# Performance work log

Hardware: AMD Instinct MI355X
Metric: run time of the kernel (lower is better)

The kernel has to match this reference:

```python
import jax, jax.numpy as jnp
import numpy as np

N_NODES = 100000
N_EDGES = 3200000
N_FEAT = 64
HID = 64
GDIM = 32
N_CLASS = 2
NUM_GRAPHS = 16


def setup_inputs() -> dict:
    key = jax.random.key(0)
    ks = jax.random.split(key, 24)

    def w(k, fan_in, fan_out):
        return (jax.random.normal(k, (fan_in, fan_out), jnp.float32) / np.sqrt(fan_in)).astype(jnp.float32)

    inp = {
        'x': jax.random.normal(ks[0], (N_NODES, N_FEAT), jnp.float32),
        'edge_index': jax.random.randint(ks[1], (2, N_EDGES), 0, N_NODES, jnp.int32),
        'batch': jnp.sort(jax.random.randint(ks[2], (N_NODES,), 0, NUM_GRAPHS, jnp.int32)),
        # lin0: nr_features -> nhid0
        'lin0_w': w(ks[3], N_FEAT, HID), 'lin0_b': jnp.zeros((HID,), jnp.float32),
        # SAGEConv 1: lin_l (aggregated, with bias), lin_r (self, no bias)
        's1_lw': w(ks[4], HID, HID), 's1_lb': jnp.zeros((HID,), jnp.float32), 's1_rw': w(ks[5], HID, HID),
        # SAGEConv 2
        's2_lw': w(ks[6], HID, HID), 's2_lb': jnp.zeros((HID,), jnp.float32), 's2_rw': w(ks[7], HID, HID),
        # embedding heads
        'emb0_w': w(ks[8], HID, GDIM), 'emb0_b': jnp.zeros((GDIM,), jnp.float32),
        'emb1_w': w(ks[9], HID, GDIM), 'emb1_b': jnp.zeros((GDIM,), jnp.float32),
        'emb2_w': w(ks[10], HID, GDIM), 'emb2_b': jnp.zeros((GDIM,), jnp.float32),
        'merge_w': w(ks[11], 3 * GDIM, GDIM), 'merge_b': jnp.zeros((GDIM,), jnp.float32),
        # global attention pooling: gate_nn (GDIM->1), v_nn (GDIM->GDIM)
        'gate_w': w(ks[12], GDIM, 1), 'gate_b': jnp.zeros((1,), jnp.float32),
        'v_w': w(ks[13], GDIM, GDIM), 'v_b': jnp.zeros((GDIM,), jnp.float32),
        'out_w': w(ks[14], GDIM, N_CLASS), 'out_b': jnp.zeros((N_CLASS,), jnp.float32),
    }
    return inp


def _sage(x, src, dst, lw, lb, rw):
    # mean aggregation of source features at destination nodes
    deg = jax.ops.segment_sum(jnp.ones_like(src, jnp.float32), dst, num_segments=N_NODES)
    agg = jax.ops.segment_sum(x[src], dst, num_segments=N_NODES)
    mean = agg / jnp.maximum(deg, 1.0)[:, None]
    return mean @ lw + lb + x @ rw


def reference(x, edge_index, batch,
              lin0_w, lin0_b, s1_lw, s1_lb, s1_rw, s2_lw, s2_lb, s2_rw,
              emb0_w, emb0_b, emb1_w, emb1_b, emb2_w, emb2_b,
              merge_w, merge_b, gate_w, gate_b, v_w, v_b, out_w, out_b):
    src, dst = edge_index[0], edge_index[1]
    x0 = x @ lin0_w + lin0_b                       # [N, HID]
    x1 = _sage(x0, src, dst, s1_lw, s1_lb, s1_rw)  # [N, HID]
    x2 = _sage(x1, src, dst, s2_lw, s2_lb, s2_rw)  # [N, HID]
    # eval mode: dropout = identity
    e0 = jax.nn.relu(x0 @ emb0_w + emb0_b)
    e1 = jax.nn.relu(x1 @ emb1_w + emb1_b)
    e2 = jax.nn.relu(x2 @ emb2_w + emb2_b)
    xc = jax.nn.relu(jnp.concatenate([e0, e1, e2], axis=1) @ merge_w + merge_b)  # [N, GDIM]
    # global attention pooling with per-graph softmax
    g = (xc @ gate_w + gate_b)[:, 0]               # [N]
    v = xc @ v_w + v_b                             # [N, GDIM]
    m = jax.ops.segment_max(g, batch, num_segments=NUM_GRAPHS)
    e = jnp.exp(g - m[batch])
    d = jax.ops.segment_sum(e, batch, num_segments=NUM_GRAPHS)
    a = e / d[batch]
    pooled = jax.ops.segment_sum(a[:, None] * v, batch, num_segments=NUM_GRAPHS)  # [NG, GDIM]
    logits = pooled @ out_w + out_b                # [NG, 2]
    output1 = jax.nn.softmax(logits, axis=-1)
    output2 = logits
    return (output1, output2)
```

## Files before the change

kernel.cpp:

```cpp
#include <hip/hip_runtime.h>
#include <hip/hip_bf16.h>
#include <hip/hip_fp16.h>

#define N_NODES 100000
#define N_EDGES 3200000
#define HID 64
#define GDIM 32
#define NUM_GRAPHS 16
#define NB1 256
#define BSHIFT 9
#define B1 512

__device__ __forceinline__ unsigned fkey(float f) {
    unsigned u = __float_as_uint(f);
    return (u & 0x80000000u) ? ~u : (u | 0x80000000u);
}
__device__ __forceinline__ float funkey(unsigned k) {
    unsigned u = (k & 0x80000000u) ? (k ^ 0x80000000u) : ~k;
    return __uint_as_float(u);
}

struct half4 { __half2 lo, hi; };
struct __align__(16) half8 { __half2 a, b, c, d; };

__global__ __launch_bounds__(256) void hist1_kernel(const int* __restrict__ dst, int* __restrict__ h1, int E4) {
    __shared__ int h[NB1];
    int t = threadIdx.x, b = blockIdx.x;
    h[t] = 0;
    __syncthreads();
    for (int i = b * 256 + t; i < E4; i += B1 * 256) {
        int4 d = ((const int4*)dst)[i];
        atomicAdd(&h[d.x >> BSHIFT], 1);
        atomicAdd(&h[d.y >> BSHIFT], 1);
        atomicAdd(&h[d.z >> BSHIFT], 1);
        atomicAdd(&h[d.w >> BSHIFT], 1);
    }
    __syncthreads();
    h1[b * NB1 + t] = h[t];
}

__global__ __launch_bounds__(256) void scan1_kernel(const int* __restrict__ h1, int* __restrict__ off1,
                                                    int* __restrict__ bstart, int E) {
    __shared__ int ts[256];
    int t = threadIdx.x;
    int tot = 0;
    for (int k = 0; k < B1; k++) tot += h1[k * NB1 + t];
    ts[t] = tot;
    __syncthreads();
    for (int off = 1; off < 256; off <<= 1) {
        int v = (t >= off) ? ts[t - off] : 0;
        __syncthreads();
        ts[t] += v;
        __syncthreads();
    }
    int base = ts[t] - tot;
    bstart[t] = base;
    if (t == 255) bstart[256] = E;
    int run = base;
    for (int k = 0; k < B1; k++) { off1[k * NB1 + t] = run; run += h1[k * NB1 + t]; }
}

__global__ __launch_bounds__(256) void scatter1_kernel(const int* __restrict__ src, const int* __restrict__ dst,
                                                       const int* __restrict__ off1, int* __restrict__ pairs, int E4) {
    __shared__ int cur[NB1];
    int t = threadIdx.x, b = blockIdx.x;
    cur[t] = off1[b * NB1 + t];
    __syncthreads();
    for (int i = b * 256 + t; i < E4; i += B1 * 256) {
        int4 d = ((const int4*)dst)[i];
        int4 s = ((const int4*)src)[i];
        int p0 = atomicAdd(&cur[d.x >> BSHIFT], 1);
        int p1 = atomicAdd(&cur[d.y >> BSHIFT], 1);
        int p2 = atomicAdd(&cur[d.z >> BSHIFT], 1);
        int p3 = atomicAdd(&cur[d.w >> BSHIFT], 1);
        pairs[p0] = (s.x << BSHIFT) | (d.x & 511);
        pairs[p1] = (s.y << BSHIFT) | (d.y & 511);
        pairs[p2] = (s.z << BSHIFT) | (d.z & 511);
        pairs[p3] = (s.w << BSHIFT) | (d.w & 511);
    }
}

__global__ __launch_bounds__(256) void bucket_csr_kernel(const int* __restrict__ pairs, const int* __restrict__ bstart,
                                                         int* __restrict__ rowstart, int* __restrict__ csr,
                                                         int N, int E) {
    __shared__ int hist[512];
    __shared__ int ts[256];
    int b = blockIdx.x, t = threadIdx.x;
    int estart = bstart[b], eend = bstart[b + 1];
    hist[t] = 0; hist[t + 256] = 0;
    __syncthreads();
    for (int e = estart + t; e < eend; e += 256) {
        int pr = pairs[e];
        atomicAdd(&hist[pr & 511], 1);
    }
    __syncthreads();
    int a0 = hist[2 * t], a1 = hist[2 * t + 1];
    int s = a0 + a1;
    ts[t] = s;
    __syncthreads();
    for (int off = 1; off < 256; off <<= 1) {
        int v = (t >= off) ? ts[t - off] : 0;
        __syncthreads();
        ts[t] += v;
        __syncthreads();
    }
    int excl = ts[t] - s;
    __syncthreads();
    hist[2 * t]     = estart + excl;
    hist[2 * t + 1] = estart + excl + a0;
    int nb0 = b << BSHIFT;
    int i0 = nb0 + 2 * t, i1 = i0 + 1;
    if (i0 < N) rowstart[i0] = estart + excl;
    if (i1 < N) rowstart[i1] = estart + excl + a0;
    if (b == gridDim.x - 1 && t == 0) rowstart[N] = E;
    __syncthreads();
    for (int e = estart + t; e < eend; e += 256) {
        int pr = pairs[e];
        int p = atomicAdd(&hist[pr & 511], 1);
        csr[p] = pr >> BSHIFT;
    }
}

__global__ __launch_bounds__(256) void lin0_kernel(const float* __restrict__ x, const float* __restrict__ W,
                            const float* __restrict__ b, float* __restrict__ y, __half* __restrict__ yh, int N) {
    __shared__ __align__(16) float Wl[64 * 64];
    __shared__ float bl[64];
    int t = threadIdx.x;
    for (int i = t; i < 64 * 64; i += 256) Wl[i] = W[i];
    if (t < 64) bl[t] = b[t];
    __syncthreads();
    int row = blockIdx.x * 256 + t;
    if (row >= N) return;
    float acc[64];
#pragma unroll
    for (int j = 0; j < 64; j++) acc[j] = bl[j];
    const float4* xr = (const float4*)(x + (size_t)row * 64);
#pragma unroll
    for (int c = 0; c < 16; c++) {
        float4 xv = xr[c];
        float xs[4] = {xv.x, xv.y, xv.z, xv.w};
#pragma unroll
        for (int kk = 0; kk < 4; kk++) {
            int k = c * 4 + kk;
#pragma unroll
            for (int j4 = 0; j4 < 16; j4++) {
                float4 w = *(const float4*)&Wl[k * 64 + j4 * 4];
                acc[j4 * 4 + 0] += xs[kk] * w.x;
                acc[j4 * 4 + 1] += xs[kk] * w.y;
                acc[j4 * 4 + 2] += xs[kk] * w.z;
                acc[j4 * 4 + 3] += xs[kk] * w.w;
            }
        }
    }
    float4* yr = (float4*)(y + (size_t)row * 64);
#pragma unroll
    for (int c = 0; c < 16; c++)
        yr[c] = make_float4(acc[c * 4], acc[c * 4 + 1], acc[c * 4 + 2], acc[c * 4 + 3]);
    __half2* hr = (__half2*)(yh + (size_t)row * 64);
#pragma unroll
    for (int c = 0; c < 32; c++)
        hr[c] = __halves2half2(__float2half_rn(acc[c * 2]), __float2half_rn(acc[c * 2 + 1]));
}

__global__ __launch_bounds__(256) void agg_kernel(const __half* __restrict__ xh, const int* __restrict__ rowstart,
                           const int* __restrict__ csr, float* __restrict__ meanout, int N) {
    int wid = threadIdx.x >> 6, lane = threadIdx.x & 63;
    int node = blockIdx.x * 4 + wid;
    if (node >= N) return;
    int ro = rowstart[node], re = rowstart[node + 1];
    int g = lane >> 3, c8 = lane & 7;
    float acc[8];
#pragma unroll
    for (int j = 0; j < 8; j++) acc[j] = 0.f;
    for (int base = ro; base < re; base += 64) {
        int rem = re - base;
        int idx = 0;
        if (lane < rem) idx = csr[base + lane];
        int kmax = rem < 64 ? rem : 64;
        for (int k = 0; k < kmax; k += 8) {
            int e = k + g;
            int s = __shfl(idx, e);
            if (e < kmax) {
                half8 hv = *(const half8*)(xh + (size_t)s * 64 + (c8 << 3));
                float2 f0 = __half22float2(hv.a);
                float2 f1 = __half22float2(hv.b);
                float2 f2 = __half22float2(hv.c);
                float2 f3 = __half22float2(hv.d);
                acc[0] += f0.x; acc[1] += f0.y; acc[2] += f1.x; acc[3] += f1.y;
                acc[4] += f2.x; acc[5] += f2.y; acc[6] += f3.x; acc[7] += f3.y;
            }
        }
    }
#pragma unroll
    for (int off = 8; off < 64; off <<= 1) {
#pragma unroll
        for (int j = 0; j < 8; j++) acc[j] += __shfl_xor(acc[j], off);
    }
    int deg = re - ro;
    float inv = 1.0f / (float)(deg > 0 ? deg : 1);
    if (lane < 8) {
        float4* mr = (float4*)(meanout + (size_t)node * 64 + (c8 << 3));
        mr[0] = make_float4(acc[0] * inv, acc[1] * inv, acc[2] * inv, acc[3] * inv);
        mr[1] = make_float4(acc[4] * inv, acc[5] * inv, acc[6] * inv, acc[7] * inv);
    }
}

__global__ __launch_bounds__(256) void sage_kernel(const float* __restrict__ mean, const float* __restrict__ xin,
                            const float* __restrict__ lw, const float* __restrict__ lb,
                            const float* __restrict__ rw, float* __restrict__ xout,
                            __half* __restrict__ xhout, int N) {
    __shared__ __align__(16) float LW[64 * 64];
    __shared__ __align__(16) float RW[64 * 64];
    __shared__ float LB[64];
    int t = threadIdx.x;
    for (int i = t; i < 64 * 64; i += 256) { LW[i] = lw[i]; RW[i] = rw[i]; }
    if (t < 64) LB[t] = lb[t];
    __syncthreads();
    int row = blockIdx.x * 256 + t;
    if (row >= N) return;
    float acc[64];
#pragma unroll
    for (int j = 0; j < 64; j++) acc[j] = LB[j];
    const float4* mr = (const float4*)(mean + (size_t)row * 64);
    const float4* xr = (const float4*)(xin + (size_t)row * 64);
#pragma unroll
    for (int c = 0; c < 16; c++) {
        float4 xv = mr[c];
        float xs[4] = {xv.x, xv.y, xv.z, xv.w};
#pragma unroll
        for (int kk = 0; kk < 4; kk++) {
            int k = c * 4 + kk;
#pragma unroll
            for (int j4 = 0; j4 < 16; j4++) {
                float4 w = *(const float4*)&LW[k * 64 + j4 * 4];
                acc[j4 * 4 + 0] += xs[kk] * w.x;
                acc[j4 * 4 + 1] += xs[kk] * w.y;
                acc[j4 * 4 + 2] += xs[kk] * w.z;
                acc[j4 * 4 + 3] += xs[kk] * w.w;
            }
        }
    }
#pragma unroll
    for (int c = 0; c < 16; c++) {
        float4 xv = xr[c];
        float xs[4] = {xv.x, xv.y, xv.z, xv.w};
#pragma unroll
        for (int kk = 0; kk < 4; kk++) {
            int k = c * 4 + kk;
#pragma unroll
            for (int j4 = 0; j4 < 16; j4++) {
                float4 w = *(const float4*)&RW[k * 64 + j4 * 4];
                acc[j4 * 4 + 0] += xs[kk] * w.x;
                acc[j4 * 4 + 1] += xs[kk] * w.y;
                acc[j4 * 4 + 2] += xs[kk] * w.z;
                acc[j4 * 4 + 3] += xs[kk] * w.w;
            }
        }
    }
    float4* yr = (float4*)(xout + (size_t)row * 64);
#pragma unroll
    for (int c = 0; c < 16; c++)
        yr[c] = make_float4(acc[c * 4], acc[c * 4 + 1], acc[c * 4 + 2], acc[c * 4 + 3]);
    if (xhout) {
        __half2* hr = (__half2*)(xhout + (size_t)row * 64);
#pragma unroll
        for (int c = 0; c < 32; c++)
            hr[c] = __halves2half2(__float2half_rn(acc[c * 2]), __float2half_rn(acc[c * 2 + 1]));
    }
}

__global__ __launch_bounds__(256) void head_kernel(const float* __restrict__ x0, const float* __restrict__ x1,
                            const float* __restrict__ x2, const int* __restrict__ batch,
                            const float* __restrict__ e0w, const float* __restrict__ e0b,
                            const float* __restrict__ e1w, const float* __restrict__ e1b,
                            const float* __restrict__ e2w, const float* __restrict__ e2b,
                            const float* __restrict__ mw, const float* __restrict__ mb,
                            const float* __restrict__ gw, const float* __restrict__ gbp,
                            const float* __restrict__ vw, const float* __restrict__ vb,
                            float* __restrict__ gout, float* __restrict__ vout,
                            unsigned* __restrict__ mkey, int N) {
    __shared__ __align__(16) float EW[3 * 64 * 32];
    __shared__ __align__(16) float MW[96 * 32];
    __shared__ __align__(16) float VW[32 * 32];
    __shared__ float EB[96], MB[32], GW[32], VB[32];
    __shared__ float GB;
    __shared__ unsigned smax[16];
    int t = threadIdx.x;
    for (int i = t; i < 2048; i += 256) { EW[i] = e0w[i]; EW[2048 + i] = e1w[i]; EW[4096 + i] = e2w[i]; }
    for (int i = t; i < 3072; i += 256) MW[i] = mw[i];
    for (int i = t; i < 1024; i += 256) VW[i] = vw[i];
    if (t < 32) { EB[t] = e0b[t]; EB[32 + t] = e1b[t]; EB[64 + t] = e2b[t];
                  MB[t] = mb[t]; GW[t] = gw[t]; VB[t] = vb[t]; }
    if (t == 0) GB = gbp[0];
    if (t < 16) smax[t] = 0u;
    __syncthreads();
    int node = blockIdx.x * 256 + t;
    if (node < N) {
        float xc[32];
#pragma unroll
        for (int j = 0; j < 32; j++) xc[j] = MB[j];
        const float* px[3] = {x0 + (size_t)node * 64, x1 + (size_t)node * 64, x2 + (size_t)node * 64};
        for (int h = 0; h < 3; h++) {
            float e[32];
#pragma unroll
            for (int j = 0; j < 32; j++) e[j] = EB[h * 32 + j];
            const float4* xr = (const float4*)px[h];
#pragma unroll
            for (int c = 0; c < 16; c++) {
                float4 xv = xr[c];
                float xs[4] = {xv.x, xv.y, xv.z, xv.w};
#pragma unroll
                for (int kk = 0; kk < 4; kk++) {
                    int k = c * 4 + kk;
#pragma unroll
                    for (int j4 = 0; j4 < 8; j4++) {
                        float4 w = *(const float4*)&EW[h * 2048 + k * 32 + j4 * 4];
                        e[j4 * 4 + 0] += xs[kk] * w.x;
                        e[j4 * 4 + 1] += xs[kk] * w.y;
                        e[j4 * 4 + 2] += xs[kk] * w.z;
                        e[j4 * 4 + 3] += xs[kk] * w.w;
                    }
                }
            }
#pragma unroll
            for (int j = 0; j < 32; j++) e[j] = fmaxf(e[j], 0.f);
#pragma unroll
            for (int i = 0; i < 32; i++) {
#pragma unroll
                for (int j4 = 0; j4 < 8; j4++) {
                    float4 w = *(const float4*)&MW[(h * 32 + i) * 32 + j4 * 4];
                    xc[j4 * 4 + 0] += e[i] * w.x;
                    xc[j4 * 4 + 1] += e[i] * w.y;
                    xc[j4 * 4 + 2] += e[i] * w.z;
                    xc[j4 * 4 + 3] += e[i] * w.w;
                }
            }
        }
#pragma unroll
        for (int j = 0; j < 32; j++) xc[j] = fmaxf(xc[j], 0.f);
        float g = GB;
#pragma unroll
        for (int i = 0; i < 32; i++) g += xc[i] * GW[i];
        float vv[32];
#pragma unroll
        for (int j = 0; j < 32; j++) vv[j] = VB[j];
#pragma unroll
        for (int i = 0; i < 32; i++) {
#pragma unroll
            for (int j4 = 0; j4 < 8; j4++) {
                float4 w = *(const float4*)&VW[i * 32 + j4 * 4];
                vv[j4 * 4 + 0] += xc[i] * w.x;
                vv[j4 * 4 + 1] += xc[i] * w.y;
                vv[j4 * 4 + 2] += xc[i] * w.z;
                vv[j4 * 4 + 3] += xc[i] * w.w;
            }
        }
        gout[node] = g;
        float4* vr = (float4*)(vout + (size_t)node * 32);
#pragma unroll
        for (int c = 0; c < 8; c++)
            vr[c] = make_float4(vv[c * 4], vv[c * 4 + 1], vv[c * 4 + 2], vv[c * 4 + 3]);
        atomicMax(&smax[batch[node]], fkey(g));
    }
    __syncthreads();
    if (t < 16) atomicMax(&mkey[t], smax[t]);
}

__global__ __launch_bounds__(256) void pool_kernel(const float* __restrict__ g, const float* __restrict__ v,
                            const int* __restrict__ batch, const unsigned* __restrict__ mkey,
                            float* __restrict__ dsum, float* __restrict__ pooled, int N) {
    __shared__ float sd[16];
    __shared__ float sp[16 * 32];
    __shared__ float sm[16];
    int t = threadIdx.x;
    if (t < 16) { sd[t] = 0.f; sm[t] = funkey(mkey[t]); }
    for (int i = t; i < 512; i += 256) sp[i] = 0.f;
    __syncthreads();
    int node = blockIdx.x * 256 + t;
    if (node < N) {
        int b = batch[node];
        float e = __expf(g[node] - sm[b]);
        atomicAdd(&sd[b], e);
        const float4* vr = (const float4*)(v + (size_t)node * 32);
#pragma unroll
        for (int c = 0; c < 8; c++) {
            float4 vv = vr[c];
            atomicAdd(&sp[b * 32 + c * 4 + 0], e * vv.x);
            atomicAdd(&sp[b * 32 + c * 4 + 1], e * vv.y);
            atomicAdd(&sp[b * 32 + c * 4 + 2], e * vv.z);
            atomicAdd(&sp[b * 32 + c * 4 + 3], e * vv.w);
        }
    }
    __syncthreads();
    if (t < 16) atomicAdd(&dsum[t], sd[t]);
    for (int i = t; i < 512; i += 256) atomicAdd(&pooled[i], sp[i]);
}

__global__ __launch_bounds__(64) void final_kernel(const float* __restrict__ dsum, const float* __restrict__ pooled,
                             const float* __restrict__ ow, const float* __restrict__ ob,
                             float* __restrict__ out) {
    int t = threadIdx.x;
    if (t >= 16) return;
    float d = dsum[t];
    float l0 = ob[0], l1 = ob[1];
    for (int i = 0; i < 32; i++) {
        float p = pooled[t * 32 + i] / d;
        l0 += p * ow[i * 2 + 0];
        l1 += p * ow[i * 2 + 1];
    }
    float m = fmaxf(l0, l1);
    float e0 = __expf(l0 - m), e1 = __expf(l1 - m);
    float s = e0 + e1;
    out[t * 2 + 0] = e0 / s;
    out[t * 2 + 1] = e1 / s;
    out[32 + t * 2 + 0] = l0;
    out[32 + t * 2 + 1] = l1;
}

extern "C" void kernel_launch(void* const* d_in, const int* in_sizes, int n_in,
                              void* d_out, int out_size, void* d_ws, size_t ws_size,
                              hipStream_t stream) {
    const float* x       = (const float*)d_in[0];
    const int*   ei      = (const int*)d_in[1];
    const int*   batch   = (const int*)d_in[2];
    const float* lin0_w  = (const float*)d_in[3];
    const float* lin0_b  = (const float*)d_in[4];
    const float* s1_lw   = (const float*)d_in[5];
    const float* s1_lb   = (const float*)d_in[6];
    const float* s1_rw   = (const float*)d_in[7];
    const float* s2_lw   = (const float*)d_in[8];
    const float* s2_lb   = (const float*)d_in[9];
    const float* s2_rw   = (const float*)d_in[10];
    const float* e0w     = (const float*)d_in[11];
    const float* e0b     = (const float*)d_in[12];
    const float* e1w     = (const float*)d_in[13];
    const float* e1b     = (const float*)d_in[14];
    const float* e2w     = (const float*)d_in[15];
    const float* e2b     = (const float*)d_in[16];
    const float* mw      = (const float*)d_in[17];
    const float* mb      = (const float*)d_in[18];
    const float* gw      = (const float*)d_in[19];
    const float* gb      = (const float*)d_in[20];
    const float* vw      = (const float*)d_in[21];
    const float* vb      = (const float*)d_in[22];
    const float* ow      = (const float*)d_in[23];
    const float* ob      = (const float*)d_in[24];
    float* out = (float*)d_out;

    const int N = N_NODES, E = N_EDGES;
    const int* src = ei;
    const int* dst = ei + E;

    char* p = (char*)d_ws;
    auto carve = [&](size_t bytes) { char* r = p; p += (bytes + 255) & ~(size_t)255; return (void*)r; };
    float* x0      = (float*)carve((size_t)N * 64 * 4);
    float* x1      = (float*)carve((size_t)N * 64 * 4);
    float* x2      = (float*)carve((size_t)N * 64 * 4);
    __half* x0h    = (__half*)carve((size_t)N * 64 * 2);
    __half* x1h    = (__half*)carve((size_t)N * 64 * 2);
    float* meanb   = (float*)carve((size_t)N * 64 * 4);
    float* vbuf    = (float*)carve((size_t)N * 32 * 4);
    float* gbuf    = (float*)carve((size_t)N * 4);
    int*   csr     = (int*)carve((size_t)E * 4);
    int*   pairs   = (int*)carve((size_t)E * 4);
    int*   h1      = (int*)carve((size_t)B1 * NB1 * 4);
    int*   off1    = (int*)carve((size_t)B1 * NB1 * 4);
    int*   bstart  = (int*)carve((NB1 + 1) * 4);
    int*   rowstart= (int*)carve((size_t)(N + 1) * 4);
    unsigned* mkey = (unsigned*)carve(16 * 4);
    float* dsum    = (float*)carve(16 * 4);
    float* pooled  = (float*)carve(16 * 32 * 4);

    hipMemsetAsync(mkey, 0, 16 * 4, stream);
    hipMemsetAsync(dsum, 0, 16 * 4, stream);
    hipMemsetAsync(pooled, 0, 16 * 32 * 4, stream);

    const int E4 = E / 4;
    int nbl = (N + 255) / 256;
    int abl = (N + 3) / 4;
    const int NBUCK = (N + 511) >> BSHIFT;

    hist1_kernel<<<B1, 256, 0, stream>>>(dst, h1, E4);
    scan1_kernel<<<1, 256, 0, stream>>>(h1, off1, bstart, E);
    scatter1_kernel<<<B1, 256, 0, stream>>>(src, dst, off1, pairs, E4);
    bucket_csr_kernel<<<NBUCK, 256, 0, stream>>>(pairs, bstart, rowstart, csr, N, E);

    lin0_kernel<<<nbl, 256, 0, stream>>>(x, lin0_w, lin0_b, x0, x0h, N);

    agg_kernel<<<abl, 256, 0, stream>>>(x0h, rowstart, csr, meanb, N);
    sage_kernel<<<nbl, 256, 0, stream>>>(meanb, x0, s1_lw, s1_lb, s1_rw, x1, x1h, N);

    agg_kernel<<<abl, 256, 0, stream>>>(x1h, rowstart, csr, meanb, N);
    sage_kernel<<<nbl, 256, 0, stream>>>(meanb, x1, s2_lw, s2_lb, s2_rw, x2, (__half*)nullptr, N);

    head_kernel<<<nbl, 256, 0, stream>>>(x0, x1, x2, batch,
                                         e0w, e0b, e1w, e1b, e2w, e2b,
                                         mw, mb, gw, gb, vw, vb,
                                         gbuf, vbuf, mkey, N);

    pool_kernel<<<nbl, 256, 0, stream>>>(gbuf, vbuf, batch, mkey, dsum, pooled, N);

    final_kernel<<<1, 64, 0, stream>>>(dsum, pooled, ow, ob, out);
}
```

Before: 508.6 us.

## Fuse second SAGE layer into head kernel and halve CSR bucket width

The second SAGE linear layer is merged into the head kernel, so x2 is kept in registers and no longer written to or read back from global memory, and one launch is dropped. Separately, the radix bucketing for CSR construction now uses 512 buckets of 256 nodes instead of 256 buckets of 512, giving more blocks in bucket_csr and a simpler per-thread scan. The fused kernel holds about 73KB of weights in shared memory plus many live registers, which could lower occupancy.

```diff
diff --git a/kernel.cpp b/kernel.cpp
--- a/kernel.cpp
+++ b/kernel.cpp
@@ -7,8 +7,8 @@
 #define HID 64
 #define GDIM 32
 #define NUM_GRAPHS 16
-#define NB1 256
-#define BSHIFT 9
+#define NB1 512
+#define BSHIFT 8
 #define B1 512
 
 __device__ __forceinline__ unsigned fkey(float f) {
@@ -26,7 +26,7 @@
 __global__ __launch_bounds__(256) void hist1_kernel(const int* __restrict__ dst, int* __restrict__ h1, int E4) {
     __shared__ int h[NB1];
     int t = threadIdx.x, b = blockIdx.x;
-    h[t] = 0;
+    h[t] = 0; h[t + 256] = 0;
     __syncthreads();
     for (int i = b * 256 + t; i < E4; i += B1 * 256) {
         int4 d = ((const int4*)dst)[i];
@@ -37,15 +37,18 @@
     }
     __syncthreads();
     h1[b * NB1 + t] = h[t];
+    h1[b * NB1 + t + 256] = h[t + 256];
 }
 
 __global__ __launch_bounds__(256) void scan1_kernel(const int* __restrict__ h1, int* __restrict__ off1,
                                                     int* __restrict__ bstart, int E) {
     __shared__ int ts[256];
     int t = threadIdx.x;
-    int tot = 0;
-    for (int k = 0; k < B1; k++) tot += h1[k * NB1 + t];
-    ts[t] = tot;
+    int b0 = 2 * t, b1 = 2 * t + 1;
+    int tot0 = 0, tot1 = 0;
+    for (int k = 0; k < B1; k++) { tot0 += h1[k * NB1 + b0]; tot1 += h1[k * NB1 + b1]; }
+    int pairtot = tot0 + tot1;
+    ts[t] = pairtot;
     __syncthreads();
     for (int off = 1; off < 256; off <<= 1) {
         int v = (t >= off) ? ts[t - off] : 0;
@@ -53,11 +56,16 @@
         ts[t] += v;
         __syncthreads();
     }
-    int base = ts[t] - tot;
-    bstart[t] = base;
-    if (t == 255) bstart[256] = E;
-    int run = base;
-    for (int k = 0; k < B1; k++) { off1[k * NB1 + t] = run; run += h1[k * NB1 + t]; }
+    int base0 = ts[t] - pairtot;
+    int base1 = base0 + tot0;
+    bstart[b0] = base0;
+    bstart[b1] = base1;
+    if (t == 255) bstart[NB1] = E;
+    int run0 = base0, run1 = base1;
+    for (int k = 0; k < B1; k++) {
+        off1[k * NB1 + b0] = run0; run0 += h1[k * NB1 + b0];
+        off1[k * NB1 + b1] = run1; run1 += h1[k * NB1 + b1];
+    }
 }
 
 __global__ __launch_bounds__(256) void scatter1_kernel(const int* __restrict__ src, const int* __restrict__ dst,
@@ -65,6 +73,7 @@
     __shared__ int cur[NB1];
     int t = threadIdx.x, b = blockIdx.x;
     cur[t] = off1[b * NB1 + t];
+    cur[t + 256] = off1[b * NB1 + t + 256];
     __syncthreads();
     for (int i = b * 256 + t; i < E4; i += B1 * 256) {
         int4 d = ((const int4*)dst)[i];
@@ -73,29 +82,28 @@
         int p1 = atomicAdd(&cur[d.y >> BSHIFT], 1);
         int p2 = atomicAdd(&cur[d.z >> BSHIFT], 1);
         int p3 = atomicAdd(&cur[d.w >> BSHIFT], 1);
-        pairs[p0] = (s.x << BSHIFT) | (d.x & 511);
-        pairs[p1] = (s.y << BSHIFT) | (d.y & 511);
-        pairs[p2] = (s.z << BSHIFT) | (d.z & 511);
-        pairs[p3] = (s.w << BSHIFT) | (d.w & 511);
+        pairs[p0] = (s.x << BSHIFT) | (d.x & 255);
+        pairs[p1] = (s.y << BSHIFT) | (d.y & 255);
+        pairs[p2] = (s.z << BSHIFT) | (d.z & 255);
+        pairs[p3] = (s.w << BSHIFT) | (d.w & 255);
     }
 }
 
 __global__ __launch_bounds__(256) void bucket_csr_kernel(const int* __restrict__ pairs, const int* __restrict__ bstart,
                                                          int* __restrict__ rowstart, int* __restrict__ csr,
                                                          int N, int E) {
-    __shared__ int hist[512];
+    __shared__ int hist[256];
     __shared__ int ts[256];
     int b = blockIdx.x, t = threadIdx.x;
     int estart = bstart[b], eend = bstart[b + 1];
-    hist[t] = 0; hist[t + 256] = 0;
+    hist[t] = 0;
     __syncthreads();
     for (int e = estart + t; e < eend; e += 256) {
         int pr = pairs[e];
-        atomicAdd(&hist[pr & 511], 1);
-    }
-    __syncthreads();
-    int a0 = hist[2 * t], a1 = hist[2 * t + 1];
-    int s = a0 + a1;
+        atomicAdd(&hist[pr & 255], 1);
+    }
+    __syncthreads();
+    int s = hist[t];
     ts[t] = s;
     __syncthreads();
     for (int off = 1; off < 256; off <<= 1) {
@@ -106,17 +114,14 @@
     }
     int excl = ts[t] - s;
     __syncthreads();
-    hist[2 * t]     = estart + excl;
-    hist[2 * t + 1] = estart + excl + a0;
-    int nb0 = b << BSHIFT;
-    int i0 = nb0 + 2 * t, i1 = i0 + 1;
+    hist[t] = estart + excl;
+    int i0 = (b << BSHIFT) + t;
     if (i0 < N) rowstart[i0] = estart + excl;
-    if (i1 < N) rowstart[i1] = estart + excl + a0;
     if (b == gridDim.x - 1 && t == 0) rowstart[N] = E;
     __syncthreads();
     for (int e = estart + t; e < eend; e += 256) {
         int pr = pairs[e];
-        int p = atomicAdd(&hist[pr & 511], 1);
+        int p = atomicAdd(&hist[pr & 255], 1);
         csr[p] = pr >> BSHIFT;
     }
 }
@@ -269,26 +274,100 @@
     }
 }
 
-__global__ __launch_bounds__(256) void head_kernel(const float* __restrict__ x0, const float* __restrict__ x1,
-                            const float* __restrict__ x2, const int* __restrict__ batch,
-                            const float* __restrict__ e0w, const float* __restrict__ e0b,
-                            const float* __restrict__ e1w, const float* __restrict__ e1b,
-                            const float* __restrict__ e2w, const float* __restrict__ e2b,
-                            const float* __restrict__ mw, const float* __restrict__ mb,
-                            const float* __restrict__ gw, const float* __restrict__ gbp,
-                            const float* __restrict__ vw, const float* __restrict__ vb,
-                            float* __restrict__ gout, float* __restrict__ vout,
-                            unsigned* __restrict__ mkey, int N) {
-    __shared__ __align__(16) float EW[3 * 64 * 32];
-    __shared__ __align__(16) float MW[96 * 32];
-    __shared__ __align__(16) float VW[32 * 32];
-    __shared__ float EB[96], MB[32], GW[32], VB[32];
+__device__ __forceinline__ void hop_accum(const float4* __restrict__ xr, const float* EWh,
+                                          const float* ebh, const float* MWh, float* xc) {
+    float e[32];
+#pragma unroll
+    for (int j = 0; j < 32; j++) e[j] = ebh[j];
+#pragma unroll
+    for (int c = 0; c < 16; c++) {
+        float4 xv = xr[c];
+        float xs[4] = {xv.x, xv.y, xv.z, xv.w};
+#pragma unroll
+        for (int kk = 0; kk < 4; kk++) {
+            int k = c * 4 + kk;
+#pragma unroll
+            for (int j4 = 0; j4 < 8; j4++) {
+                float4 w = *(const float4*)&EWh[k * 32 + j4 * 4];
+                e[j4 * 4 + 0] += xs[kk] * w.x;
+                e[j4 * 4 + 1] += xs[kk] * w.y;
+                e[j4 * 4 + 2] += xs[kk] * w.z;
+                e[j4 * 4 + 3] += xs[kk] * w.w;
+            }
+        }
+    }
+#pragma unroll
+    for (int j = 0; j < 32; j++) e[j] = fmaxf(e[j], 0.f);
+#pragma unroll
+    for (int i = 0; i < 32; i++) {
+#pragma unroll
+        for (int j4 = 0; j4 < 8; j4++) {
+            float4 w = *(const float4*)&MWh[i * 32 + j4 * 4];
+            xc[j4 * 4 + 0] += e[i] * w.x;
+            xc[j4 * 4 + 1] += e[i] * w.y;
+            xc[j4 * 4 + 2] += e[i] * w.z;
+            xc[j4 * 4 + 3] += e[i] * w.w;
+        }
+    }
+}
+
+__device__ __forceinline__ void hop_accum_reg(const float* a64, const float* EWh,
+                                              const float* ebh, const float* MWh, float* xc) {
+    float e[32];
+#pragma unroll
+    for (int j = 0; j < 32; j++) e[j] = ebh[j];
+#pragma unroll
+    for (int k = 0; k < 64; k++) {
+#pragma unroll
+        for (int j4 = 0; j4 < 8; j4++) {
+            float4 w = *(const float4*)&EWh[k * 32 + j4 * 4];
+            e[j4 * 4 + 0] += a64[k] * w.x;
+            e[j4 * 4 + 1] += a64[k] * w.y;
+            e[j4 * 4 + 2] += a64[k] * w.z;
+            e[j4 * 4 + 3] += a64[k] * w.w;
+        }
+    }
+#pragma unroll
+    for (int j = 0; j < 32; j++) e[j] = fmaxf(e[j], 0.f);
+#pragma unroll
+    for (int i = 0; i < 32; i++) {
+#pragma unroll
+        for (int j4 = 0; j4 < 8; j4++) {
+            float4 w = *(const float4*)&MWh[i * 32 + j4 * 4];
+            xc[j4 * 4 + 0] += e[i] * w.x;
+            xc[j4 * 4 + 1] += e[i] * w.y;
+            xc[j4 * 4 + 2] += e[i] * w.z;
+            xc[j4 * 4 + 3] += e[i] * w.w;
+        }
+    }
+}
+
+__global__ __launch_bounds__(256) void sagehead_kernel(
+    const float* __restrict__ mean, const float* __restrict__ x0, const float* __restrict__ x1,
+    const float* __restrict__ lw, const float* __restrict__ lb, const float* __restrict__ rw,
+    const int* __restrict__ batch,
+    const float* __restrict__ e0w, const float* __restrict__ e0b,
+    const float* __restrict__ e1w, const float* __restrict__ e1b,
+    const float* __restrict__ e2w, const float* __restrict__ e2b,
+    const float* __restrict__ mw, const float* __restrict__ mb,
+    const float* __restrict__ gw, const float* __restrict__ gbp,
+    const float* __restrict__ vw, const float* __restrict__ vb,
+    float* __restrict__ gout, float* __restrict__ vout,
+    unsigned* __restrict__ mkey, int N) {
+    __shared__ __align__(16) float LW[4096];
+    __shared__ __align__(16) float RW[4096];
+    __shared__ __align__(16) float EW[6144];
+    __shared__ __align__(16) float MW[3072];
+    __shared__ __align__(16) float VW[1024];
+    __shared__ float LB[64], EB[96], MB[32], GW[32], VB[32];
     __shared__ float GB;
     __shared__ unsigned smax[16];
     int t = threadIdx.x;
+    for (int i = t; i < 4096; i += 256) { LW[i] = lw[i]; RW[i] = rw[i]; }
     for (int i = t; i < 2048; i += 256) { EW[i] = e0w[i]; EW[2048 + i] = e1w[i]; EW[4096 + i] = e2w[i]; }
     for (int i = t; i < 3072; i += 256) MW[i] = mw[i];
     for (int i = t; i < 1024; i += 256) VW[i] = vw[i];
+    if (t < 64) LB[t] = lb[t];
     if (t < 32) { EB[t] = e0b[t]; EB[32 + t] = e1b[t]; EB[64 + t] = e2b[t];
                   MB[t] = mb[t]; GW[t] = gw[t]; VB[t] = vb[t]; }
     if (t == 0) GB = gbp[0];
@@ -296,46 +375,51 @@
     __syncthreads();
     int node = blockIdx.x * 256 + t;
     if (node < N) {
+        float acc[64];
+#pragma unroll
+        for (int j = 0; j < 64; j++) acc[j] = LB[j];
+        const float4* mr = (const float4*)(mean + (size_t)node * 64);
+        const float4* xr1 = (const float4*)(x1 + (size_t)node * 64);
+#pragma unroll
+        for (int c = 0; c < 16; c++) {
+            float4 xv = mr[c];
+            float xs[4] = {xv.x, xv.y, xv.z, xv.w};
+#pragma unroll
+            for (int kk = 0; kk < 4; kk++) {
+                int k = c * 4 + kk;
+#pragma unroll
+                for (int j4 = 0; j4 < 16; j4++) {
+                    float4 w = *(const float4*)&LW[k * 64 + j4 * 4];
+                    acc[j4 * 4 + 0] += xs[kk] * w.x;
+                    acc[j4 * 4 + 1] += xs[kk] * w.y;
+                    acc[j4 * 4 + 2] += xs[kk] * w.z;
+                    acc[j4 * 4 + 3] += xs[kk] * w.w;
+                }
+            }
+        }
+#pragma unroll
+        for (int c = 0; c < 16; c++) {
+            float4 xv = xr1[c];
+            float xs[4] = {xv.x, xv.y, xv.z, xv.w};
+#pragma unroll
+            for (int kk = 0; kk < 4; kk++) {
+                int k = c * 4 + kk;
+#pragma unroll
+                for (int j4 = 0; j4 < 16; j4++) {
+                    float4 w = *(const float4*)&RW[k * 64 + j4 * 4];
+                    acc[j4 * 4 + 0] += xs[kk] * w.x;
+                    acc[j4 * 4 + 1] += xs[kk] * w.y;
+                    acc[j4 * 4 + 2] += xs[kk] * w.z;
+                    acc[j4 * 4 + 3] += xs[kk] * w.w;
+                }
+            }
+        }
         float xc[32];
 #pragma unroll
         for (int j = 0; j < 32; j++) xc[j] = MB[j];
-        const float* px[3] = {x0 + (size_t)node * 64, x1 + (size_t)node * 64, x2 + (size_t)node * 64};
-        for (int h = 0; h < 3; h++) {
-            float e[32];
-#pragma unroll
-            for (int j = 0; j < 32; j++) e[j] = EB[h * 32 + j];
-            const float4* xr = (const float4*)px[h];
-#pragma unroll
-            for (int c = 0; c < 16; c++) {
-                float4 xv = xr[c];
-                float xs[4] = {xv.x, xv.y, xv.z, xv.w};
-#pragma unroll
-                for (int kk = 0; kk < 4; kk++) {
-                    int k = c * 4 + kk;
-#pragma unroll
-                    for (int j4 = 0; j4 < 8; j4++) {
-                        float4 w = *(const float4*)&EW[h * 2048 + k * 32 + j4 * 4];
-                        e[j4 * 4 + 0] += xs[kk] * w.x;
-                        e[j4 * 4 + 1] += xs[kk] * w.y;
-                        e[j4 * 4 + 2] += xs[kk] * w.z;
-                        e[j4 * 4 + 3] += xs[kk] * w.w;
-                    }
-                }
-            }
-#pragma unroll
-            for (int j = 0; j < 32; j++) e[j] = fmaxf(e[j], 0.f);
-#pragma unroll
-            for (int i = 0; i < 32; i++) {
-#pragma unroll
-                for (int j4 = 0; j4 < 8; j4++) {
-                    float4 w = *(const float4*)&MW[(h * 32 + i) * 32 + j4 * 4];
-                    xc[j4 * 4 + 0] += e[i] * w.x;
-                    xc[j4 * 4 + 1] += e[i] * w.y;
-                    xc[j4 * 4 + 2] += e[i] * w.z;
-                    xc[j4 * 4 + 3] += e[i] * w.w;
-                }
-            }
-        }
+        hop_accum((const float4*)(x0 + (size_t)node * 64), &EW[0],    &EB[0],  &MW[0],    xc);
+        hop_accum((const float4*)(x1 + (size_t)node * 64), &EW[2048], &EB[32], &MW[1024], xc);
+        hop_accum_reg(acc,                                  &EW[4096], &EB[64], &MW[2048], xc);
 #pragma unroll
         for (int j = 0; j < 32; j++) xc[j] = fmaxf(xc[j], 0.f);
         float g = GB;
@@ -455,7 +539,6 @@
     auto carve = [&](size_t bytes) { char* r = p; p += (bytes + 255) & ~(size_t)255; return (void*)r; };
     float* x0      = (float*)carve((size_t)N * 64 * 4);
     float* x1      = (float*)carve((size_t)N * 64 * 4);
-    float* x2      = (float*)carve((size_t)N * 64 * 4);
     __half* x0h    = (__half*)carve((size_t)N * 64 * 2);
     __half* x1h    = (__half*)carve((size_t)N * 64 * 2);
     float* meanb   = (float*)carve((size_t)N * 64 * 4);
@@ -478,7 +561,7 @@
     const int E4 = E / 4;
     int nbl = (N + 255) / 256;
     int abl = (N + 3) / 4;
-    const int NBUCK = (N + 511) >> BSHIFT;
+    const int NBUCK = (N + 255) >> BSHIFT;
 
     hist1_kernel<<<B1, 256, 0, stream>>>(dst, h1, E4);
     scan1_kernel<<<1, 256, 0, stream>>>(h1, off1, bstart, E);
@@ -491,12 +574,12 @@
     sage_kernel<<<nbl, 256, 0, stream>>>(meanb, x0, s1_lw, s1_lb, s1_rw, x1, x1h, N);
 
     agg_kernel<<<abl, 256, 0, stream>>>(x1h, rowstart, csr, meanb, N);
-    sage_kernel<<<nbl, 256, 0, stream>>>(meanb, x1, s2_lw, s2_lb, s2_rw, x2, (__half*)nullptr, N);
-
-    head_kernel<<<nbl, 256, 0, stream>>>(x0, x1, x2, batch,
-                                         e0w, e0b, e1w, e1b, e2w, e2b,
-                                         mw, mb, gw, gb, vw, vb,
-                                         gbuf, vbuf, mkey, N);
+
+    sagehead_kernel<<<nbl, 256, 0, stream>>>(meanb, x0, x1,
+                                             s2_lw, s2_lb, s2_rw, batch,
+                                             e0w, e0b, e1w, e1b, e2w, e2b,
+                                             mw, mb, gw, gb, vw, vb,
+                                             gbuf, vbuf, mkey, N);
 
     pool_kernel<<<nbl, 256, 0, stream>>>(gbuf, vbuf, batch, mkey, dsum, pooled, N);
 
```

Result: slower. 649.7 us (+27.7%).
